# Kernel tuning notes

Hardware: AMD Instinct MI355X
Metric: run time of the kernel (lower is better)

The kernel has to match this reference:

```python
import jax, jax.numpy as jnp
import numpy as np

EPS = 1e-12  # torch F.normalize default eps

def _l2norm(x):
    # F.normalize(x, dim=1): x / max(||x||, eps)
    n = jnp.sqrt(jnp.sum(x * x, axis=1, keepdims=True))
    return x / jnp.maximum(n, EPS)

def setup_inputs() -> dict:
    key = jax.random.key(0)
    k1, k2 = jax.random.split(key)
    B, M, D = 4096, 8192, 1024
    query = jax.random.normal(k1, (B, D), dtype=jnp.float32)
    memory = jax.random.normal(k2, (M, D), dtype=jnp.float32)
    return {"query": query, "memory": memory}

def reference(query, memory):
    # memory buffer is normalized at construction time
    mem = _l2norm(memory)              # [M, D]
    q = _l2norm(query)                 # [B, D]
    sim = jnp.einsum('bd,md->bm', q, mem)          # [B, M] cosine similarity
    attn = jax.nn.softmax(sim, axis=1)             # [B, M]
    memory_features = jnp.einsum('bm,md->bd', attn, mem)  # [B, D]
    return (memory_features, attn)
```

## Files before the change

### kernel.cpp

```cpp
#include <hip/hip_runtime.h>
#include <stdint.h>

#define NB 4096
#define NM 8192
#define ND 1024

typedef __attribute__((ext_vector_type(8))) short bf16x8;
typedef __attribute__((ext_vector_type(4))) float f32x4;
typedef __attribute__((ext_vector_type(8))) unsigned short u16x8;
typedef __attribute__((ext_vector_type(4))) int i32x4;
typedef __attribute__((ext_vector_type(8))) int i32x8;

#define SCONE 0x7F7F7F7F

static __device__ __forceinline__ unsigned short f2bf(float f) {
  union { float f; uint32_t u; } v; v.f = f;
  uint32_t u = v.u;
  u += 0x7fffu + ((u >> 16) & 1u);
  return (unsigned short)(u >> 16);
}
static __device__ __forceinline__ float bf2f(unsigned short b) {
  union { uint32_t u; float f; } v; v.u = ((uint32_t)b) << 16; return v.f;
}
static __device__ __forceinline__ uint8_t f2fp8(float f) {
  union { float f; uint32_t u; } v; v.f = f;
  const uint8_t s = (uint8_t)((v.u >> 31) << 7);
  const float a = fabsf(f);
  if (a >= 448.f) return s | 0x7E;
  if (a < 0.0009765625f) return s;
  const uint32_t u = v.u & 0x7FFFFFFFu;
  const int e = (int)(u >> 23) - 127;
  if (e < -6) {
    int m = (int)rintf(a * 512.f);
    if (m >= 8) return s | 0x08;
    return s | (uint8_t)m;
  }
  const uint32_t r = u + 0x7FFFFu + ((u >> 20) & 1u);
  const int e2 = (int)(r >> 23) - 127;
  if (e2 > 8) return s | 0x7E;
  return s | (uint8_t)((e2 + 7) << 3) | (uint8_t)((r >> 20) & 7u);
}

static __device__ __forceinline__ void gload_lds16(const void* g, void* l) {
  __builtin_amdgcn_global_load_lds(
      (__attribute__((address_space(1))) void*)g,
      (__attribute__((address_space(3))) void*)l, 16, 0, 0);
}

#define BAR()   __builtin_amdgcn_s_barrier()
#define LGKM0() asm volatile("s_waitcnt lgkmcnt(0)" ::: "memory")
#define VMC8()  asm volatile("s_waitcnt vmcnt(8)" ::: "memory")
#define VMC2()  asm volatile("s_waitcnt vmcnt(2)" ::: "memory")
#define VMC0()  asm volatile("s_waitcnt vmcnt(0)" ::: "memory")

__global__ void nrm_m8(const float* __restrict__ x, unsigned short* __restrict__ ob,
                       uint8_t* __restrict__ o8) {
  const int row = blockIdx.x, t = threadIdx.x;
  const float4 v = ((const float4*)(x + (size_t)row * ND))[t];
  float ss = v.x * v.x + v.y * v.y + v.z * v.z + v.w * v.w;
  #pragma unroll
  for (int o = 32; o > 0; o >>= 1) ss += __shfl_xor(ss, o);
  __shared__ float red[4];
  if ((t & 63) == 0) red[t >> 6] = ss;
  __syncthreads();
  ss = (red[0] + red[1]) + (red[2] + red[3]);
  const float sc = 1.0f / fmaxf(sqrtf(ss), 1e-12f);
  ushort4 o4;
  o4.x = f2bf(v.x * sc); o4.y = f2bf(v.y * sc);
  o4.z = f2bf(v.z * sc); o4.w = f2bf(v.w * sc);
  ((ushort4*)(ob + (size_t)row * ND))[t] = o4;
  uchar4 c4;
  c4.x = f2fp8(v.x * sc); c4.y = f2fp8(v.y * sc);
  c4.z = f2fp8(v.z * sc); c4.w = f2fp8(v.w * sc);
  ((uchar4*)(o8 + (size_t)row * ND))[t] = c4;
}

__global__ void nrm_q8(const float* __restrict__ x, uint8_t* __restrict__ o8) {
  const int row = blockIdx.x, t = threadIdx.x;
  const float4 v = ((const float4*)(x + (size_t)row * ND))[t];
  float ss = v.x * v.x + v.y * v.y + v.z * v.z + v.w * v.w;
  #pragma unroll
  for (int o = 32; o > 0; o >>= 1) ss += __shfl_xor(ss, o);
  __shared__ float red[4];
  if ((t & 63) == 0) red[t >> 6] = ss;
  __syncthreads();
  ss = (red[0] + red[1]) + (red[2] + red[3]);
  const float sc = 1.0f / fmaxf(sqrtf(ss), 1e-12f);
  uchar4 c4;
  c4.x = f2fp8(v.x * sc); c4.y = f2fp8(v.y * sc);
  c4.z = f2fp8(v.z * sc); c4.w = f2fp8(v.w * sc);
  ((uchar4*)(o8 + (size_t)row * ND))[t] = c4;
}

__global__ void tr_kernel(const unsigned short* __restrict__ memn, unsigned short* __restrict__ memt) {
  __shared__ unsigned short Ts[64][66];
  const int t = threadIdx.x;
  const int d0 = blockIdx.x * 64, m0 = blockIdx.y * 64;
  #pragma unroll
  for (int r = 0; r < 2; ++r) {
    const int lrow = r * 32 + (t >> 3);
    const int lcol = (t & 7) * 8;
    u16x8 v = *(const u16x8*)(memn + (size_t)(m0 + lrow) * ND + d0 + lcol);
    #pragma unroll
    for (int j = 0; j < 8; ++j) Ts[lcol + j][lrow] = v[j];
  }
  __syncthreads();
  #pragma unroll
  for (int r = 0; r < 2; ++r) {
    const int orow = r * 32 + (t >> 3);
    const int ocol = (t & 7) * 8;
    u16x8 o;
    #pragma unroll
    for (int j = 0; j < 8; ++j) o[j] = Ts[orow][ocol + j];
    *(u16x8*)(memt + (size_t)(d0 + orow) * NM + m0 + ocol) = o;
  }
}

__global__ __launch_bounds__(512, 2) void gemm4x(
    const uint8_t* __restrict__ A, const uint8_t* __restrict__ B,
    unsigned short* __restrict__ E, float* __restrict__ psum,
    int ld, int ldc, int mt, int kchunk)
{
  extern __shared__ char smem[];
  const int t = threadIdx.x;
  const int w = t >> 6, l = t & 63;
  const int wr = w >> 2, wc = w & 3;
  const int nwg = gridDim.x, cpx = nwg >> 3;
  const int id = (blockIdx.x & 7) * cpx + (blockIdx.x >> 3);
  const int brow = id % mt, bcol = id / mt;
  const int nt = kchunk >> 7;

  const int srow = l >> 3;
  const int scol = ((l & 7) ^ srow) << 4;
  const int lr = l & 15, lhi = l >> 4;
  const int swz = (l & 7) << 4;
  const int cb0 = (lhi * 32) ^ swz;
  const int cb1 = (lhi * 32 + 16) ^ swz;
  const int aoffr = (wr * 16 + lr) * 128;
  const int boffr = (wc * 16 + lr) * 128;

  const uint8_t* Ab = A + (size_t)(brow * 256 + w * 8 + srow) * ld + scol;
  const uint8_t* Bb = B + (size_t)(bcol * 256 + w * 8 + srow) * ld + scol;

  auto stageA = [&](int p, int h, int tau) {
    const int kt = (tau < nt ? tau : nt - 1) << 7;
    const uint8_t* g = Ab + (size_t)(h * 128) * ld + kt;
    char* d = smem + p * 65536 + h * 16384 + w * 1024;
    gload_lds16(g, d);
    gload_lds16(g + (size_t)64 * ld, d + 8192);
  };
  auto stageB = [&](int p, int h, int tau) {
    const int kt = (tau < nt ? tau : nt - 1) << 7;
    const uint8_t* g = Bb + (size_t)(h * 128) * ld + kt;
    char* d = smem + p * 65536 + 32768 + h * 16384 + w * 1024;
    gload_lds16(g, d);
    gload_lds16(g + (size_t)64 * ld, d + 8192);
  };
  auto ldA4 = [&](int p, int m, int c) -> i32x4 {
    return *(const i32x4*)(smem + p * 65536 + m * 4096 + aoffr + (c ? cb1 : cb0));
  };
  auto ldB4 = [&](int p, int nf, int c) -> i32x4 {
    return *(const i32x4*)(smem + p * 65536 + 32768 + nf * 8192 + boffr + (c ? cb1 : cb0));
  };

  f32x4 acc[8][4] = {};
  i32x8 alo[4], ahi[4], bloA[2], bloB[2], bhi[2];

  #define RDA4(DST, P, MB)                                                     \
    _Pragma("unroll")                                                          \
    for (int m_ = 0; m_ < 4; ++m_) {                                           \
      i32x4 lo_ = ldA4(P, (MB) + m_, 0), hi_ = ldA4(P, (MB) + m_, 1);          \
      i32x8 r_; r_[0]=lo_[0]; r_[1]=lo_[1]; r_[2]=lo_[2]; r_[3]=lo_[3];        \
      r_[4]=hi_[0]; r_[5]=hi_[1]; r_[6]=hi_[2]; r_[7]=hi_[3]; DST[m_] = r_; }
  #define RDB4(DST, P, NBASE)                                                  \
    _Pragma("unroll")                                                          \
    for (int n_ = 0; n_ < 2; ++n_) {                                           \
      i32x4 lo_ = ldB4(P, (NBASE) + n_, 0), hi_ = ldB4(P, (NBASE) + n_, 1);    \
      i32x8 r_; r_[0]=lo_[0]; r_[1]=lo_[1]; r_[2]=lo_[2]; r_[3]=lo_[3];        \
      r_[4]=hi_[0]; r_[5]=hi_[1]; r_[6]=hi_[2]; r_[7]=hi_[3]; DST[n_] = r_; }
  #define CL8(AF, BF, MO, NO)                                                  \
    __builtin_amdgcn_s_setprio(1);                                             \
    _Pragma("unroll")                                                          \
    for (int m_ = 0; m_ < 4; ++m_)                                             \
      _Pragma("unroll")                                                        \
      for (int n_ = 0; n_ < 2; ++n_)                                           \
        acc[(MO) + m_][(NO) + n_] =                                            \
            __builtin_amdgcn_mfma_scale_f32_16x16x128_f8f6f4(                  \
                AF[m_], BF[n_], acc[(MO) + m_][(NO) + n_],                     \
                0, 0, 0, SCONE, 0, SCONE);                                     \
    __builtin_amdgcn_s_setprio(0);

  stageA(0, 0, 0); stageA(0, 1, 0); stageB(0, 0, 0); stageB(0, 1, 0);
  stageA(1, 0, 1); stageA(1, 1, 1); stageB(1, 0, 1); stageB(1, 1, 1);
  VMC8();
  BAR();
  RDA4(alo, 0, 0);
  RDB4(bloA, 0, 0);

  const int niter = nt >> 1;
  for (int i = 0; i < niter; ++i) {
    const int t2 = 2 * i + 2, t3 = 2 * i + 3;
    LGKM0();
    CL8(alo, bloA, 0, 0);
    RDB4(bhi, 0, 2);
    BAR();
    LGKM0();
    CL8(alo, bhi, 0, 2);
    RDA4(ahi, 0, 4);
    stageB(0, 0, t2);
    VMC2();
    BAR();
    LGKM0();
    CL8(ahi, bhi, 4, 2);
    RDB4(bloB, 1, 0);
    stageB(0, 1, t2); stageA(0, 0, t2);
    BAR();
    LGKM0();
    CL8(ahi, bloA, 4, 0);
    RDA4(alo, 1, 0);
    stageA(0, 1, t2);
    BAR();
    LGKM0();
    CL8(alo, bloB, 0, 0);
    RDB4(bhi, 1, 2);
    BAR();
    LGKM0();
    CL8(alo, bhi, 0, 2);
    RDA4(ahi, 1, 4);
    stageB(1, 0, t3);
    VMC2();
    BAR();
    LGKM0();
    CL8(ahi, bhi, 4, 2);
    RDB4(bloA, 0, 0);
    stageB(1, 1, t3); stageA(1, 0, t3);
    BAR();
    LGKM0();
    CL8(ahi, bloB, 4, 0);
    RDA4(alo, 0, 0);
    stageA(1, 1, t3);
    BAR();
  }
  #undef RDA4
  #undef RDB4
  #undef CL8

  const int crow0 = brow * 256 + wr * 16 + lhi * 4;
  const int ccol0 = bcol * 256 + wc * 16 + lr;
  float rs[8][4];
  #pragma unroll
  for (int m = 0; m < 8; ++m)
    #pragma unroll
    for (int j = 0; j < 4; ++j) rs[m][j] = 0.f;
  #pragma unroll
  for (int m = 0; m < 8; ++m)
    #pragma unroll
    for (int n = 0; n < 4; ++n)
      #pragma unroll
      for (int j = 0; j < 4; ++j) {
        const float e = __expf(acc[m][n][j]);
        rs[m][j] += e;
        E[(size_t)(crow0 + m * 32 + j) * ldc + ccol0 + n * 64] = f2bf(e);
      }
  #pragma unroll
  for (int m = 0; m < 8; ++m)
    #pragma unroll
    for (int j = 0; j < 4; ++j)
      #pragma unroll
      for (int o = 1; o < 16; o <<= 1) rs[m][j] += __shfl_xor(rs[m][j], o);
  VMC0();
  __syncthreads();
  float* ls = (float*)smem;
  if (lr == 0) {
    #pragma unroll
    for (int m = 0; m < 8; ++m)
      #pragma unroll
      for (int j = 0; j < 4; ++j)
        ls[wc * 256 + wr * 16 + m * 32 + lhi * 4 + j] = rs[m][j];
  }
  __syncthreads();
  if (t < 256) {
    const float s4 = ls[t] + ls[256 + t] + ls[512 + t] + ls[768 + t];
    psum[(size_t)bcol * NB + brow * 256 + t] = s4;
  }
}

__global__ void sinv_kernel(const float* __restrict__ psum, float* __restrict__ sinv) {
  const int row = blockIdx.x * 256 + threadIdx.x;
  float s = 0.f;
  #pragma unroll
  for (int k = 0; k < 32; ++k) s += psum[(size_t)k * NB + row];
  sinv[row] = 1.0f / s;
}

__global__ __launch_bounds__(512, 2) void gemm4r(
    const unsigned short* __restrict__ A, const unsigned short* __restrict__ B,
    float* __restrict__ C, const float* __restrict__ sinvp,
    float* __restrict__ attnp, int ld, int ldc, int mt, int tps, int kchunk,
    unsigned long long cstride)
{
  extern __shared__ char smem[];
  const int t = threadIdx.x;
  const int w = t >> 6, l = t & 63;
  const int wr = w >> 2, wc = w & 3;
  const int nwg = gridDim.x, cpx = nwg >> 3;
  const int id = (blockIdx.x & 7) * cpx + (blockIdx.x >> 3);
  const int ksp = id / tps, rem = id % tps;
  const int brow = rem % mt, bcol = rem / mt;
  const int k0 = ksp * kchunk;
  const int nt = kchunk >> 6;

  const int srow = l >> 3;
  const int scol = ((l & 7) ^ srow) << 3;
  const int lr = l & 15, lhi = l >> 4;
  const int swz = (l & 7) << 4;
  const int cbk0 = (lhi * 16) ^ swz;
  const int cbk1 = (64 + lhi * 16) ^ swz;
  const int aoffr = (wr * 16 + lr) * 128;
  const int boffr = (wc * 16 + lr) * 128;

  const unsigned short* Ab = A + (size_t)(brow * 256 + w * 8 + srow) * ld + k0 + scol;
  const unsigned short* Bb = B + (size_t)(bcol * 256 + w * 8 + srow) * ld + k0 + scol;

  auto stageA = [&](int p, int h, int tau) {
    const int kt = (tau < nt ? tau : nt - 1) << 6;
    const unsigned short* g = Ab + (size_t)(h * 128) * ld + kt;
    char* d = smem + p * 65536 + h * 16384 + w * 1024;
    gload_lds16(g, d);
    gload_lds16(g + (size_t)64 * ld, d + 8192);
  };
  auto stageB = [&](int p, int h, int tau) {
    const int kt = (tau < nt ? tau : nt - 1) << 6;
    const unsigned short* g = Bb + (size_t)(h * 128) * ld + kt;
    char* d = smem + p * 65536 + 32768 + h * 16384 + w * 1024;
    gload_lds16(g, d);
    gload_lds16(g + (size_t)64 * ld, d + 8192);
  };
  auto ldA = [&](int p, int m, int kk) -> bf16x8 {
    return *(const bf16x8*)(smem + p * 65536 + m * 4096 + aoffr + (kk ? cbk1 : cbk0));
  };
  auto ldB = [&](int p, int nf, int kk) -> bf16x8 {
    return *(const bf16x8*)(smem + p * 65536 + 32768 + nf * 8192 + boffr + (kk ? cbk1 : cbk0));
  };

  f32x4 acc[8][4] = {};
  bf16x8 alo[4][2], ahi[4][2], bloA[2][2], bloB[2][2], bhi[2][2];

  stageA(0, 0, 0); stageA(0, 1, 0); stageB(0, 0, 0); stageB(0, 1, 0);
  stageA(1, 0, 1); stageA(1, 1, 1); stageB(1, 0, 1); stageB(1, 1, 1);
  VMC8();
  BAR();
  #pragma unroll
  for (int m = 0; m < 4; ++m) { alo[m][0] = ldA(0, m, 0); alo[m][1] = ldA(0, m, 1); }
  #pragma unroll
  for (int n = 0; n < 2; ++n) { bloA[n][0] = ldB(0, n, 0); bloA[n][1] = ldB(0, n, 1); }

  #define CL(AF, BF, MO, NO)                                                   \
    __builtin_amdgcn_s_setprio(1);                                             \
    _Pragma("unroll")                                                          \
    for (int kk = 0; kk < 2; ++kk)                                             \
      _Pragma("unroll")                                                        \
      for (int m = 0; m < 4; ++m)                                              \
        _Pragma("unroll")                                                      \
        for (int n = 0; n < 2; ++n)                                            \
          acc[MO + m][NO + n] = __builtin_amdgcn_mfma_f32_16x16x32_bf16(       \
              AF[m][kk], BF[n][kk], acc[MO + m][NO + n], 0, 0, 0);             \
    __builtin_amdgcn_s_setprio(0);

  const int niter = nt >> 1;
  for (int i = 0; i < niter; ++i) {
    const int t2 = 2 * i + 2, t3 = 2 * i + 3;
    LGKM0();
    CL(alo, bloA, 0, 0);
    #pragma unroll
    for (int n = 0; n < 2; ++n) { bhi[n][0] = ldB(0, 2 + n, 0); bhi[n][1] = ldB(0, 2 + n, 1); }
    BAR();
    LGKM0();
    CL(alo, bhi, 0, 2);
    #pragma unroll
    for (int m = 0; m < 4; ++m) { ahi[m][0] = ldA(0, 4 + m, 0); ahi[m][1] = ldA(0, 4 + m, 1); }
    stageB(0, 0, t2);
    VMC2();
    BAR();
    LGKM0();
    CL(ahi, bhi, 4, 2);
    #pragma unroll
    for (int n = 0; n < 2; ++n) { bloB[n][0] = ldB(1, n, 0); bloB[n][1] = ldB(1, n, 1); }
    stageB(0, 1, t2); stageA(0, 0, t2);
    BAR();
    LGKM0();
    CL(ahi, bloA, 4, 0);
    #pragma unroll
    for (int m = 0; m < 4; ++m) { alo[m][0] = ldA(1, m, 0); alo[m][1] = ldA(1, m, 1); }
    stageA(0, 1, t2);
    BAR();
    LGKM0();
    CL(alo, bloB, 0, 0);
    #pragma unroll
    for (int n = 0; n < 2; ++n) { bhi[n][0] = ldB(1, 2 + n, 0); bhi[n][1] = ldB(1, 2 + n, 1); }
    BAR();
    LGKM0();
    CL(alo, bhi, 0, 2);
    #pragma unroll
    for (int m = 0; m < 4; ++m) { ahi[m][0] = ldA(1, 4 + m, 0); ahi[m][1] = ldA(1, 4 + m, 1); }
    stageB(1, 0, t3);
    VMC2();
    BAR();
    LGKM0();
    CL(ahi, bhi, 4, 2);
    #pragma unroll
    for (int n = 0; n < 2; ++n) { bloA[n][0] = ldB(0, n, 0); bloA[n][1] = ldB(0, n, 1); }
    stageB(1, 1, t3); stageA(1, 0, t3);
    BAR();
    LGKM0();
    CL(ahi, bloB, 4, 0);
    #pragma unroll
    for (int m = 0; m < 4; ++m) { alo[m][0] = ldA(0, m, 0); alo[m][1] = ldA(0, m, 1); }
    stageA(1, 1, t3);
    BAR();
  }
  #undef CL

  const int crow0 = brow * 256 + wr * 16 + lhi * 4;
  const int ccol0 = bcol * 256 + wc * 16 + lr;
  float* Cp = C + (unsigned long long)ksp * cstride;
  #pragma unroll
  for (int m = 0; m < 8; ++m)
    #pragma unroll
    for (int n = 0; n < 4; ++n)
      #pragma unroll
      for (int j = 0; j < 4; ++j)
        Cp[(size_t)(crow0 + m * 32 + j) * ldc + ccol0 + n * 64] = acc[m][n][j];

  {
    const int r0 = brow * 256 + bcol * 64;
    const int nch = kchunk >> 3;
    for (int idx = t; idx < 64 * nch; idx += 512) {
      const int row = idx / nch, ch = idx % nch;
      const float inv = sinvp[r0 + row];
      u16x8 bv = *(const u16x8*)(A + (size_t)(r0 + row) * ld + k0 + ch * 8);
      float4 f0, f1;
      #pragma unroll
      for (int j = 0; j < 8; ++j) {
        const float a = bf2f(bv[j]) * inv;
        if (j < 4) (&f0.x)[j] = a; else (&f1.x)[j - 4] = a;
      }
      float* arow = attnp + (size_t)(r0 + row) * NM + k0 + ch * 8;
      *(float4*)arow = f0;
      *(float4*)(arow + 4) = f1;
    }
  }
}

__global__ void reduce_kernel(const float4* __restrict__ part, float4* __restrict__ mf,
                              const float* __restrict__ sinv) {
  const size_t n4 = (size_t)NB * ND / 4;
  for (size_t i = (size_t)blockIdx.x * blockDim.x + threadIdx.x; i < n4;
       i += (size_t)gridDim.x * blockDim.x) {
    const float is = sinv[i >> 8];
    float4 s = part[i];
    #pragma unroll
    for (int k = 1; k < 4; ++k) {
      float4 p = part[(size_t)k * n4 + i];
      s.x += p.x; s.y += p.y; s.z += p.z; s.w += p.w;
    }
    s.x *= is; s.y *= is; s.z *= is; s.w *= is;
    mf[i] = s;
  }
}

extern "C" void kernel_launch(void* const* d_in, const int* in_sizes, int n_in,
                              void* d_out, int out_size, void* d_ws, size_t ws_size,
                              hipStream_t stream) {
  const float* q   = (const float*)d_in[0];
  const float* mem = (const float*)d_in[1];
  float* mf   = (float*)d_out;
  float* attn = (float*)d_out + (size_t)NB * ND;
  char* ws = (char*)d_ws;
  uint8_t* memn8       = (uint8_t*)(ws);
  unsigned short* memn = (unsigned short*)(ws + ((size_t)8  << 20));
  unsigned short* memt = (unsigned short*)(ws + ((size_t)24 << 20));
  unsigned short* E    = (unsigned short*)(ws + ((size_t)40 << 20));
  float* psum          = (float*)(ws + ((size_t)104 << 20));
  float* sinv          = (float*)(ws + ((size_t)104 << 20) + (512 << 10));
  float* part          = (float*)(ws + ((size_t)105 << 20));
  uint8_t* qn8         = (uint8_t*)(ws + ((size_t)105 << 20));

  hipFuncSetAttribute((const void*)gemm4x,
                      hipFuncAttributeMaxDynamicSharedMemorySize, 131072);
  hipFuncSetAttribute((const void*)gemm4r,
                      hipFuncAttributeMaxDynamicSharedMemorySize, 131072);

  hipLaunchKernelGGL(nrm_m8, dim3(NM), dim3(256), 0, stream, mem, memn, memn8);
  hipLaunchKernelGGL(nrm_q8, dim3(NB), dim3(256), 0, stream, q, qn8);
  hipLaunchKernelGGL(tr_kernel, dim3(ND / 64, NM / 64), dim3(256), 0, stream, memn, memt);

  hipLaunchKernelGGL(gemm4x, dim3((NB / 256) * (NM / 256)), dim3(512), 131072, stream,
                     qn8, memn8, E, psum, ND, NM, NB / 256, ND);

  hipLaunchKernelGGL(sinv_kernel, dim3(NB / 256), dim3(256), 0, stream, psum, sinv);

  const int tps = (NB / 256) * (ND / 256);
  hipLaunchKernelGGL(gemm4r, dim3(tps * 4), dim3(512), 131072, stream,
                     E, memt, part, sinv, attn, NM, ND, NB / 256, tps, NM / 4,
                     (unsigned long long)NB * ND);
  hipLaunchKernelGGL(reduce_kernel, dim3(2048), dim3(256), 0, stream,
                     (const float4*)part, (float4*)mf, sinv);
}
```

Baseline: 187.6 us.

## Run second GEMM in FP8 using offset-encoded exp values and column-sum correction

The second GEMM (attn × mem) switches from bf16 to FP8 MFMA with block scaling. The exp scores are stored as fp8 of 16·(e−1), so values that cluster near 1 keep precision. A per-column sum of the normalized memory is added back in the reduce step to undo the offset. This halves the bytes staged for E and memT and doubles MFMA throughput, at the cost of reduced accuracy in both attn and memory_features plus two small extra colsum kernels.

```diff
diff --git a/kernel.cpp b/kernel.cpp
--- a/kernel.cpp
+++ b/kernel.cpp
@@ -12,6 +12,7 @@
 typedef __attribute__((ext_vector_type(8))) int i32x8;
 
 #define SCONE 0x7F7F7F7F
+#define SCQ16 0x7B7B7B7B
 
 static __device__ __forceinline__ unsigned short f2bf(float f) {
   union { float f; uint32_t u; } v; v.f = f;
@@ -39,6 +40,14 @@
   const int e2 = (int)(r >> 23) - 127;
   if (e2 > 8) return s | 0x7E;
   return s | (uint8_t)((e2 + 7) << 3) | (uint8_t)((r >> 20) & 7u);
+}
+static __device__ __forceinline__ float fp82f(uint8_t b) {
+  const float sgn = (b & 0x80) ? -1.f : 1.f;
+  const int e = (b >> 3) & 0xF, m = b & 7;
+  if (e == 0) return sgn * (float)m * 0.001953125f;
+  union { uint32_t u; float f; } v;
+  v.u = ((uint32_t)(e + 120) << 23) | ((uint32_t)m << 20);
+  return sgn * v.f;
 }
 
 static __device__ __forceinline__ void gload_lds16(const void* g, void* l) {
@@ -92,7 +101,7 @@
   ((uchar4*)(o8 + (size_t)row * ND))[t] = c4;
 }
 
-__global__ void tr_kernel(const unsigned short* __restrict__ memn, unsigned short* __restrict__ memt) {
+__global__ void tr8_kernel(const unsigned short* __restrict__ memn, uint8_t* __restrict__ memt8) {
   __shared__ unsigned short Ts[64][66];
   const int t = threadIdx.x;
   const int d0 = blockIdx.x * 64, m0 = blockIdx.y * 64;
@@ -109,16 +118,33 @@
   for (int r = 0; r < 2; ++r) {
     const int orow = r * 32 + (t >> 3);
     const int ocol = (t & 7) * 8;
-    u16x8 o;
-    #pragma unroll
-    for (int j = 0; j < 8; ++j) o[j] = Ts[orow][ocol + j];
-    *(u16x8*)(memt + (size_t)(d0 + orow) * NM + m0 + ocol) = o;
-  }
+    unsigned long long o = 0;
+    #pragma unroll
+    for (int j = 0; j < 8; ++j)
+      o |= (unsigned long long)f2fp8(bf2f(Ts[orow][ocol + j])) << (8 * j);
+    *(unsigned long long*)(memt8 + (size_t)(d0 + orow) * NM + m0 + ocol) = o;
+  }
+}
+
+__global__ void colsum_part(const unsigned short* __restrict__ memn, float* __restrict__ colpart) {
+  const int d = blockIdx.x * 256 + threadIdx.x;
+  const int bm = blockIdx.y;
+  float s = 0.f;
+  for (int r = 0; r < 256; ++r)
+    s += bf2f(memn[(size_t)(bm * 256 + r) * ND + d]);
+  colpart[bm * ND + d] = s;
+}
+__global__ void colred(const float* __restrict__ colpart, float* __restrict__ colsum) {
+  const int d = blockIdx.x * 256 + threadIdx.x;
+  float s = 0.f;
+  #pragma unroll
+  for (int k = 0; k < 32; ++k) s += colpart[k * ND + d];
+  colsum[d] = s;
 }
 
 __global__ __launch_bounds__(512, 2) void gemm4x(
     const uint8_t* __restrict__ A, const uint8_t* __restrict__ B,
-    unsigned short* __restrict__ E, float* __restrict__ psum,
+    uint8_t* __restrict__ X8, float* __restrict__ psum,
     int ld, int ldc, int mt, int kchunk)
 {
   extern __shared__ char smem[];
@@ -260,7 +286,7 @@
       for (int j = 0; j < 4; ++j) {
         const float e = __expf(acc[m][n][j]);
         rs[m][j] += e;
-        E[(size_t)(crow0 + m * 32 + j) * ldc + ccol0 + n * 64] = f2bf(e);
+        X8[(size_t)(crow0 + m * 32 + j) * ldc + ccol0 + n * 64] = f2fp8(16.f * (e - 1.f));
       }
   #pragma unroll
   for (int m = 0; m < 8; ++m)
@@ -293,8 +319,8 @@
   sinv[row] = 1.0f / s;
 }
 
-__global__ __launch_bounds__(512, 2) void gemm4r(
-    const unsigned short* __restrict__ A, const unsigned short* __restrict__ B,
+__global__ __launch_bounds__(512, 2) void gemm4y(
+    const uint8_t* __restrict__ A, const uint8_t* __restrict__ B,
     float* __restrict__ C, const float* __restrict__ sinvp,
     float* __restrict__ attnp, int ld, int ldc, int mt, int tps, int kchunk,
     unsigned long long cstride)
@@ -308,118 +334,122 @@
   const int ksp = id / tps, rem = id % tps;
   const int brow = rem % mt, bcol = rem / mt;
   const int k0 = ksp * kchunk;
-  const int nt = kchunk >> 6;
+  const int nt = kchunk >> 7;
 
   const int srow = l >> 3;
-  const int scol = ((l & 7) ^ srow) << 3;
+  const int scol = ((l & 7) ^ srow) << 4;
   const int lr = l & 15, lhi = l >> 4;
   const int swz = (l & 7) << 4;
-  const int cbk0 = (lhi * 16) ^ swz;
-  const int cbk1 = (64 + lhi * 16) ^ swz;
+  const int cb0 = (lhi * 32) ^ swz;
+  const int cb1 = (lhi * 32 + 16) ^ swz;
   const int aoffr = (wr * 16 + lr) * 128;
   const int boffr = (wc * 16 + lr) * 128;
 
-  const unsigned short* Ab = A + (size_t)(brow * 256 + w * 8 + srow) * ld + k0 + scol;
-  const unsigned short* Bb = B + (size_t)(bcol * 256 + w * 8 + srow) * ld + k0 + scol;
+  const uint8_t* Ab = A + (size_t)(brow * 256 + w * 8 + srow) * ld + k0 + scol;
+  const uint8_t* Bb = B + (size_t)(bcol * 256 + w * 8 + srow) * ld + k0 + scol;
 
   auto stageA = [&](int p, int h, int tau) {
-    const int kt = (tau < nt ? tau : nt - 1) << 6;
-    const unsigned short* g = Ab + (size_t)(h * 128) * ld + kt;
+    const int kt = (tau < nt ? tau : nt - 1) << 7;
+    const uint8_t* g = Ab + (size_t)(h * 128) * ld + kt;
     char* d = smem + p * 65536 + h * 16384 + w * 1024;
     gload_lds16(g, d);
     gload_lds16(g + (size_t)64 * ld, d + 8192);
   };
   auto stageB = [&](int p, int h, int tau) {
-    const int kt = (tau < nt ? tau : nt - 1) << 6;
-    const unsigned short* g = Bb + (size_t)(h * 128) * ld + kt;
+    const int kt = (tau < nt ? tau : nt - 1) << 7;
+    const uint8_t* g = Bb + (size_t)(h * 128) * ld + kt;
     char* d = smem + p * 65536 + 32768 + h * 16384 + w * 1024;
     gload_lds16(g, d);
     gload_lds16(g + (size_t)64 * ld, d + 8192);
   };
-  auto ldA = [&](int p, int m, int kk) -> bf16x8 {
-    return *(const bf16x8*)(smem + p * 65536 + m * 4096 + aoffr + (kk ? cbk1 : cbk0));
-  };
-  auto ldB = [&](int p, int nf, int kk) -> bf16x8 {
-    return *(const bf16x8*)(smem + p * 65536 + 32768 + nf * 8192 + boffr + (kk ? cbk1 : cbk0));
+  auto ldA4 = [&](int p, int m, int c) -> i32x4 {
+    return *(const i32x4*)(smem + p * 65536 + m * 4096 + aoffr + (c ? cb1 : cb0));
+  };
+  auto ldB4 = [&](int p, int nf, int c) -> i32x4 {
+    return *(const i32x4*)(smem + p * 65536 + 32768 + nf * 8192 + boffr + (c ? cb1 : cb0));
   };
 
   f32x4 acc[8][4] = {};
-  bf16x8 alo[4][2], ahi[4][2], bloA[2][2], bloB[2][2], bhi[2][2];
+  i32x8 alo[4], ahi[4], bloA[2], bloB[2], bhi[2];
+
+  #define RDA4(DST, P, MB)                                                     \
+    _Pragma("unroll")                                                          \
+    for (int m_ = 0; m_ < 4; ++m_) {                                           \
+      i32x4 lo_ = ldA4(P, (MB) + m_, 0), hi_ = ldA4(P, (MB) + m_, 1);          \
+      i32x8 r_; r_[0]=lo_[0]; r_[1]=lo_[1]; r_[2]=lo_[2]; r_[3]=lo_[3];        \
+      r_[4]=hi_[0]; r_[5]=hi_[1]; r_[6]=hi_[2]; r_[7]=hi_[3]; DST[m_] = r_; }
+  #define RDB4(DST, P, NBASE)                                                  \
+    _Pragma("unroll")                                                          \
+    for (int n_ = 0; n_ < 2; ++n_) {                                           \
+      i32x4 lo_ = ldB4(P, (NBASE) + n_, 0), hi_ = ldB4(P, (NBASE) + n_, 1);    \
+      i32x8 r_; r_[0]=lo_[0]; r_[1]=lo_[1]; r_[2]=lo_[2]; r_[3]=lo_[3];        \
+      r_[4]=hi_[0]; r_[5]=hi_[1]; r_[6]=hi_[2]; r_[7]=hi_[3]; DST[n_] = r_; }
+  #define CL8(AF, BF, MO, NO)                                                  \
+    __builtin_amdgcn_s_setprio(1);                                             \
+    _Pragma("unroll")                                                          \
+    for (int m_ = 0; m_ < 4; ++m_)                                             \
+      _Pragma("unroll")                                                        \
+      for (int n_ = 0; n_ < 2; ++n_)                                           \
+        acc[(MO) + m_][(NO) + n_] =                                            \
+            __builtin_amdgcn_mfma_scale_f32_16x16x128_f8f6f4(                  \
+                AF[m_], BF[n_], acc[(MO) + m_][(NO) + n_],                     \
+                0, 0, 0, SCQ16, 0, SCONE);                                     \
+    __builtin_amdgcn_s_setprio(0);
 
   stageA(0, 0, 0); stageA(0, 1, 0); stageB(0, 0, 0); stageB(0, 1, 0);
   stageA(1, 0, 1); stageA(1, 1, 1); stageB(1, 0, 1); stageB(1, 1, 1);
   VMC8();
   BAR();
-  #pragma unroll
-  for (int m = 0; m < 4; ++m) { alo[m][0] = ldA(0, m, 0); alo[m][1] = ldA(0, m, 1); }
-  #pragma unroll
-  for (int n = 0; n < 2; ++n) { bloA[n][0] = ldB(0, n, 0); bloA[n][1] = ldB(0, n, 1); }
-
-  #define CL(AF, BF, MO, NO)                                                   \
-    __builtin_amdgcn_s_setprio(1);                                             \
-    _Pragma("unroll")                                                          \
-    for (int kk = 0; kk < 2; ++kk)                                             \
-      _Pragma("unroll")                                                        \
-      for (int m = 0; m < 4; ++m)                                              \
-        _Pragma("unroll")                                                      \
-        for (int n = 0; n < 2; ++n)                                            \
-          acc[MO + m][NO + n] = __builtin_amdgcn_mfma_f32_16x16x32_bf16(       \
-              AF[m][kk], BF[n][kk], acc[MO + m][NO + n], 0, 0, 0);             \
-    __builtin_amdgcn_s_setprio(0);
+  RDA4(alo, 0, 0);
+  RDB4(bloA, 0, 0);
 
   const int niter = nt >> 1;
   for (int i = 0; i < niter; ++i) {
     const int t2 = 2 * i + 2, t3 = 2 * i + 3;
     LGKM0();
-    CL(alo, bloA, 0, 0);
-    #pragma unroll
-    for (int n = 0; n < 2; ++n) { bhi[n][0] = ldB(0, 2 + n, 0); bhi[n][1] = ldB(0, 2 + n, 1); }
-    BAR();
-    LGKM0();
-    CL(alo, bhi, 0, 2);
-    #pragma unroll
-    for (int m = 0; m < 4; ++m) { ahi[m][0] = ldA(0, 4 + m, 0); ahi[m][1] = ldA(0, 4 + m, 1); }
+    CL8(alo, bloA, 0, 0);
+    RDB4(bhi, 0, 2);
+    BAR();
+    LGKM0();
+    CL8(alo, bhi, 0, 2);
+    RDA4(ahi, 0, 4);
     stageB(0, 0, t2);
     VMC2();
     BAR();
     LGKM0();
-    CL(ahi, bhi, 4, 2);
-    #pragma unroll
-    for (int n = 0; n < 2; ++n) { bloB[n][0] = ldB(1, n, 0); bloB[n][1] = ldB(1, n, 1); }
+    CL8(ahi, bhi, 4, 2);
+    RDB4(bloB, 1, 0);
     stageB(0, 1, t2); stageA(0, 0, t2);
     BAR();
     LGKM0();
-    CL(ahi, bloA, 4, 0);
-    #pragma unroll
-    for (int m = 0; m < 4; ++m) { alo[m][0] = ldA(1, m, 0); alo[m][1] = ldA(1, m, 1); }
+    CL8(ahi, bloA, 4, 0);
+    RDA4(alo, 1, 0);
     stageA(0, 1, t2);
     BAR();
     LGKM0();
-    CL(alo, bloB, 0, 0);
-    #pragma unroll
-    for (int n = 0; n < 2; ++n) { bhi[n][0] = ldB(1, 2 + n, 0); bhi[n][1] = ldB(1, 2 + n, 1); }
-    BAR();
-    LGKM0();
-    CL(alo, bhi, 0, 2);
-    #pragma unroll
-    for (int m = 0; m < 4; ++m) { ahi[m][0] = ldA(1, 4 + m, 0); ahi[m][1] = ldA(1, 4 + m, 1); }
+    CL8(alo, bloB, 0, 0);
+    RDB4(bhi, 1, 2);
+    BAR();
+    LGKM0();
+    CL8(alo, bhi, 0, 2);
+    RDA4(ahi, 1, 4);
     stageB(1, 0, t3);
     VMC2();
     BAR();
     LGKM0();
-    CL(ahi, bhi, 4, 2);
-    #pragma unroll
-    for (int n = 0; n < 2; ++n) { bloA[n][0] = ldB(0, n, 0); bloA[n][1] = ldB(0, n, 1); }
+    CL8(ahi, bhi, 4, 2);
+    RDB4(bloA, 0, 0);
     stageB(1, 1, t3); stageA(1, 0, t3);
     BAR();
     LGKM0();
-    CL(ahi, bloB, 4, 0);
-    #pragma unroll
-    for (int m = 0; m < 4; ++m) { alo[m][0] = ldA(0, m, 0); alo[m][1] = ldA(0, m, 1); }
+    CL8(ahi, bloB, 4, 0);
+    RDA4(alo, 0, 0);
     stageA(1, 1, t3);
     BAR();
   }
-  #undef CL
+  #undef RDA4
+  #undef RDB4
+  #undef CL8
 
   const int crow0 = brow * 256 + wr * 16 + lhi * 4;
   const int ccol0 = bcol * 256 + wc * 16 + lr;
@@ -438,11 +468,13 @@
     for (int idx = t; idx < 64 * nch; idx += 512) {
       const int row = idx / nch, ch = idx % nch;
       const float inv = sinvp[r0 + row];
-      u16x8 bv = *(const u16x8*)(A + (size_t)(r0 + row) * ld + k0 + ch * 8);
+      const unsigned long long bv =
+          *(const unsigned long long*)(A + (size_t)(r0 + row) * ld + k0 + ch * 8);
       float4 f0, f1;
       #pragma unroll
       for (int j = 0; j < 8; ++j) {
-        const float a = bf2f(bv[j]) * inv;
+        const float x = fp82f((uint8_t)(bv >> (8 * j)));
+        const float a = (1.f + 0.0625f * x) * inv;
         if (j < 4) (&f0.x)[j] = a; else (&f1.x)[j - 4] = a;
       }
       float* arow = attnp + (size_t)(r0 + row) * NM + k0 + ch * 8;
@@ -453,18 +485,21 @@
 }
 
 __global__ void reduce_kernel(const float4* __restrict__ part, float4* __restrict__ mf,
-                              const float* __restrict__ sinv) {
+                              const float* __restrict__ sinv,
+                              const float* __restrict__ colsum) {
   const size_t n4 = (size_t)NB * ND / 4;
   for (size_t i = (size_t)blockIdx.x * blockDim.x + threadIdx.x; i < n4;
        i += (size_t)gridDim.x * blockDim.x) {
     const float is = sinv[i >> 8];
+    const float4 c4 = ((const float4*)colsum)[i & 255];
     float4 s = part[i];
     #pragma unroll
     for (int k = 1; k < 4; ++k) {
       float4 p = part[(size_t)k * n4 + i];
       s.x += p.x; s.y += p.y; s.z += p.z; s.w += p.w;
     }
-    s.x *= is; s.y *= is; s.z *= is; s.w *= is;
+    s.x = (s.x + c4.x) * is; s.y = (s.y + c4.y) * is;
+    s.z = (s.z + c4.z) * is; s.w = (s.w + c4.w) * is;
     mf[i] = s;
   }
 }
@@ -479,31 +514,35 @@
   char* ws = (char*)d_ws;
   uint8_t* memn8       = (uint8_t*)(ws);
   unsigned short* memn = (unsigned short*)(ws + ((size_t)8  << 20));
-  unsigned short* memt = (unsigned short*)(ws + ((size_t)24 << 20));
-  unsigned short* E    = (unsigned short*)(ws + ((size_t)40 << 20));
-  float* psum          = (float*)(ws + ((size_t)104 << 20));
-  float* sinv          = (float*)(ws + ((size_t)104 << 20) + (512 << 10));
-  float* part          = (float*)(ws + ((size_t)105 << 20));
-  uint8_t* qn8         = (uint8_t*)(ws + ((size_t)105 << 20));
+  uint8_t* memt8       = (uint8_t*)(ws + ((size_t)24 << 20));
+  uint8_t* X8          = (uint8_t*)(ws + ((size_t)32 << 20));
+  float* psum          = (float*)(ws + ((size_t)64 << 20));
+  float* sinv          = (float*)(ws + ((size_t)64 << 20) + (512 << 10));
+  float* colpart       = (float*)(ws + ((size_t)65 << 20));
+  float* colsum        = (float*)(ws + ((size_t)65 << 20) + (512 << 10));
+  float* part          = (float*)(ws + ((size_t)66 << 20));
+  uint8_t* qn8         = (uint8_t*)(ws + ((size_t)130 << 20));
 
   hipFuncSetAttribute((const void*)gemm4x,
                       hipFuncAttributeMaxDynamicSharedMemorySize, 131072);
-  hipFuncSetAttribute((const void*)gemm4r,
+  hipFuncSetAttribute((const void*)gemm4y,
                       hipFuncAttributeMaxDynamicSharedMemorySize, 131072);
 
   hipLaunchKernelGGL(nrm_m8, dim3(NM), dim3(256), 0, stream, mem, memn, memn8);
   hipLaunchKernelGGL(nrm_q8, dim3(NB), dim3(256), 0, stream, q, qn8);
-  hipLaunchKernelGGL(tr_kernel, dim3(ND / 64, NM / 64), dim3(256), 0, stream, memn, memt);
+  hipLaunchKernelGGL(tr8_kernel, dim3(ND / 64, NM / 64), dim3(256), 0, stream, memn, memt8);
+  hipLaunchKernelGGL(colsum_part, dim3(4, 32), dim3(256), 0, stream, memn, colpart);
+  hipLaunchKernelGGL(colred, dim3(4), dim3(256), 0, stream, colpart, colsum);
 
   hipLaunchKernelGGL(gemm4x, dim3((NB / 256) * (NM / 256)), dim3(512), 131072, stream,
-                     qn8, memn8, E, psum, ND, NM, NB / 256, ND);
+                     qn8, memn8, X8, psum, ND, NM, NB / 256, ND);
 
   hipLaunchKernelGGL(sinv_kernel, dim3(NB / 256), dim3(256), 0, stream, psum, sinv);
 
   const int tps = (NB / 256) * (ND / 256);
-  hipLaunchKernelGGL(gemm4r, dim3(tps * 4), dim3(512), 131072, stream,
-                     E, memt, part, sinv, attn, NM, ND, NB / 256, tps, NM / 4,
+  hipLaunchKernelGGL(gemm4y, dim3(tps * 4), dim3(512), 131072, stream,
+                     X8, memt8, part, sinv, attn, NM, ND, NB / 256, tps, NM / 4,
                      (unsigned long long)NB * ND);
   hipLaunchKernelGGL(reduce_kernel, dim3(2048), dim3(256), 0, stream,
-                     (const float4*)part, (float4*)mf, sinv);
-}
+                     (const float4*)part, (float4*)mf, sinv, colsum);
+}
```

Measured after the change: 246.0 us. 31.1% more time.
